# Performance work log

Measured on AMD Instinct MI355X. Metric: run time of the kernel, lower is better.

The kernel has to match this reference:

```python
import jax, jax.numpy as jnp
import numpy as np

ALPHA = 50.0
EPS = 1e-12  # torch F.normalize eps


def setup_inputs() -> dict:
    key = jax.random.key(0)
    k1, k2 = jax.random.split(key)
    N, C, H, W_sp, K = 64, 128, 64, 64, 64
    x = jax.random.normal(k1, (N, C, H, W_sp), dtype=jnp.float32)
    # centroids.permute(1,0): shape [C, K]; orthogonal-ish init approximated by scaled gaussian
    W = jax.random.normal(k2, (C, K), dtype=jnp.float32) * (1.0 / np.sqrt(C))
    bias = jnp.zeros((K,), dtype=jnp.float32)
    return {"x": x, "W": W, "bias": bias}


def _l2norm(v, axis):
    return v / jnp.maximum(jnp.linalg.norm(v, axis=axis, keepdims=True), EPS)


def reference(x, W, bias):
    N, C, H, W_sp = x.shape
    K = W.shape[1]
    x = _l2norm(x, axis=1)                      # normalize over channels
    xf = x.reshape(N, C, H * W_sp)              # [N, C, P]
    Wn = _l2norm(W, axis=0)                     # column-normalized weight [C, K]
    # soft assignment logits, computed directly in [N, K, P] layout
    sa_logits = jnp.einsum('ncp,ck->nkp', xf, Wn)
    sa = jax.nn.softmax((sa_logits + bias[None, :, None]) * ALPHA, axis=1)  # over clusters
    # VLAD via two GEMM-like contractions instead of the [N,K,C,P] residual tensor:
    # vlad[n,k,c] = sum_p sa[n,k,p] * xf[n,c,p] - W[c,k] * sum_p sa[n,k,p]
    vlad = jnp.einsum('nkp,ncp->nkc', sa, xf) - sa.sum(axis=-1)[:, :, None] * W.T[None]
    vlad = _l2norm(vlad, axis=2)                # intra-normalize per cluster
    vlad = vlad.reshape(N, K * C)
    vlad = _l2norm(vlad, axis=1)                # global L2
    return (vlad, sa_logits)                    # original returns soft_assign_ permuted to [N, K, P]
```

## Files before the change

kernel.cpp:

```cpp
#include <hip/hip_runtime.h>
#include <math.h>

#define ALPHA 50.0f
#define EPS 1e-12f

constexpr int N = 64, C = 128, P = 4096, K = 64;
constexpr int NCH2 = 8;

typedef short short8_t __attribute__((ext_vector_type(8)));
typedef short short4_t __attribute__((ext_vector_type(4)));
typedef float f4 __attribute__((ext_vector_type(4)));
typedef unsigned int u32x4 __attribute__((ext_vector_type(4)));
typedef unsigned int u32x2 __attribute__((ext_vector_type(2)));

__device__ __forceinline__ unsigned short f2bf(float f) {
    union { float f; unsigned u; } v; v.f = f;
    unsigned r = (v.u + 0x7FFFu + ((v.u >> 16) & 1u)) >> 16;
    return (unsigned short)r;
}

__device__ __forceinline__ unsigned cvtpk(float lo, float hi) {
    unsigned r;
    asm("v_cvt_pk_bf16_f32 %0, %1, %2" : "=v"(r) : "v"(lo), "v"(hi));
    return r;
}

__device__ __forceinline__ void bar_lds() {
    asm volatile("s_waitcnt lgkmcnt(0)" ::: "memory");
    __builtin_amdgcn_s_barrier();
}

__global__ __launch_bounds__(256, 2) void k_fused(
    const float* __restrict__ x, const float* __restrict__ W,
    const float* __restrict__ bias, float* __restrict__ logits,
    float* __restrict__ vlad_part, float* __restrict__ Spart,
    float* __restrict__ ss2acc)
{
    __shared__ __align__(16) char smem[71424];
    unsigned short* xsT  = (unsigned short*)smem;
    float*          saf  = (float*)smem;
    unsigned short* sa2s = (unsigned short*)(smem + 56320);
    float*          denom= (float*)(smem + 65536);
    float*          invs = (float*)(smem + 69888);
    float*          biass= (float*)(smem + 70144);
    float*          red  = (float*)(smem + 70400);
    float*          Wl   = (float*)smem;

    const int tid  = threadIdx.x;
    const int n    = blockIdx.x >> 3;
    const int blk8 = blockIdx.x & 7;
    const int pbase = blk8 * 512;

    const int w = tid >> 6, lane = tid & 63;
    const int q = lane >> 4, l15 = lane & 15;
    const int pxg = tid & 15, cg = tid >> 4;

    if (blockIdx.x == 0 && tid < 64) ss2acc[tid] = 0.f;
    if (tid < K) biass[tid] = bias[tid] * ALPHA;

    const float* xrow = x + (size_t)n * C * P + pbase + 4 * pxg;
    float4 va[8], vb[8];
    short8_t af[4];

    {
        float4 wv[8];
        #pragma unroll
        for (int it = 0; it < 8; ++it)
            wv[it] = *(const float4*)&W[(size_t)(tid + it * 256) * 4];
        #pragma unroll
        for (int j = 0; j < 8; ++j)
            va[j] = *(const float4*)&xrow[(size_t)(8 * cg + j) * P];
        #pragma unroll
        for (int it = 0; it < 8; ++it) {
            const int idx4 = tid + it * 256;
            *(float4*)&Wl[(idx4 >> 4) * 68 + (idx4 & 15) * 4] = wv[it];
        }
        bar_lds();
        {
            const int k = tid & 63, part = tid >> 6;
            float s = 0.f;
            #pragma unroll
            for (int i = 0; i < 32; ++i) {
                float v = Wl[(part * 32 + i) * 68 + k];
                s = fmaf(v, v, s);
            }
            red[tid] = s;
        }
        bar_lds();
        if (tid < 64)
            invs[tid] = 1.0f / fmaxf(
                sqrtf(red[tid] + red[64 + tid] + red[128 + tid] + red[192 + tid]), EPS);
        bar_lds();
        {
            const float cv = invs[16 * w + l15];
            #pragma unroll
            for (int c0 = 0; c0 < 4; ++c0)
                #pragma unroll
                for (int j = 0; j < 8; ++j)
                    af[c0][j] = (short)f2bf(
                        Wl[(c0 * 32 + 8 * q + j) * 68 + 16 * w + l15] * cv);
        }
        bar_lds();
    }

    f4 acc2[8];
    #pragma unroll
    for (int ct = 0; ct < 8; ++ct) acc2[ct] = (f4){0.f, 0.f, 0.f, 0.f};
    float Sreg = 0.f;

    const int pbT8 = 8 * (cg ^ (pxg & 7));
    const int l4 = l15 >> 2;

    for (int ch = 0; ch < 8; ++ch) {
        if (ch < 7) {
            const float* xb = xrow + (ch + 1) * 64;
            #pragma unroll
            for (int j = 0; j < 8; ++j)
                vb[j] = *(const float4*)&xb[(size_t)(8 * cg + j) * P];
        }
        if (ch > 0) {
            const unsigned short* xsNr =
                (const unsigned short*)(smem + 17408 + 19456 * ((ch - 1) & 1));
            short8_t a2[2];
            #pragma unroll
            for (int kit = 0; kit < 2; ++kit)
                a2[kit] = *(const short8_t*)&sa2s[(16 * w + l15) * 72 + kit * 32 + 8 * q];
            __builtin_amdgcn_s_setprio(1);
            #pragma unroll
            for (int ct = 0; ct < 8; ++ct)
                #pragma unroll
                for (int kit = 0; kit < 2; ++kit) {
                    const unsigned short* bp = &xsNr[(ct * 16 + l15) * 76 + kit * 32 + 8 * q];
                    short4_t b0 = *(const short4_t*)bp;
                    short4_t b1 = *(const short4_t*)(bp + 4);
                    short8_t bb;
                    bb[0] = b0[0]; bb[1] = b0[1]; bb[2] = b0[2]; bb[3] = b0[3];
                    bb[4] = b1[0]; bb[5] = b1[1]; bb[6] = b1[2]; bb[7] = b1[3];
                    acc2[ct] = __builtin_amdgcn_mfma_f32_16x16x32_bf16(a2[kit], bb, acc2[ct], 0, 0, 0);
                }
            __builtin_amdgcn_s_setprio(0);
        }
        {
            unsigned short* xsNw = (unsigned short*)(smem + 17408 + 19456 * (ch & 1));
            const float* vf = (const float*)va;
            float pss[4] = {0.f, 0.f, 0.f, 0.f};
            #pragma unroll
            for (int j = 0; j < 8; ++j)
                #pragma unroll
                for (int i = 0; i < 4; ++i)
                    pss[i] = fmaf(vf[j * 4 + i], vf[j * 4 + i], pss[i]);
            float* rd2 = denom;
            #pragma unroll
            for (int i = 0; i < 4; ++i) rd2[(4 * pxg + i) * 17 + cg] = pss[i];

            #pragma unroll
            for (int i = 0; i < 4; ++i) {
                u32x4 t;
                #pragma unroll
                for (int jj = 0; jj < 4; ++jj)
                    t[jj] = cvtpk(vf[(2 * jj) * 4 + i], vf[(2 * jj + 1) * 4 + i]);
                *(u32x4*)&xsT[(4 * pxg + i) * 136 + pbT8] = t;
            }
            #pragma unroll
            for (int j = 0; j < 8; ++j) {
                u32x2 t2;
                t2[0] = cvtpk(vf[j * 4 + 0], vf[j * 4 + 1]);
                t2[1] = cvtpk(vf[j * 4 + 2], vf[j * 4 + 3]);
                *(u32x2*)&xsNw[(8 * cg + j) * 76 + 4 * pxg] = t2;
            }
        }
        bar_lds();

        if (tid < 64) {
            const float* rd2 = denom;
            float s = 0.f;
            #pragma unroll
            for (int g = 0; g < 16; ++g) s += rd2[tid * 17 + g];
            invs[tid] = 1.0f / fmaxf(sqrtf(s), EPS);
        }
        f4 acc1[4];
        #pragma unroll
        for (int t = 0; t < 4; ++t) acc1[t] = (f4){0.f, 0.f, 0.f, 0.f};
        __builtin_amdgcn_s_setprio(1);
        #pragma unroll
        for (int c0 = 0; c0 < 4; ++c0)
            #pragma unroll
            for (int pxt = 0; pxt < 4; ++pxt) {
                const int pb = (4 * c0 + q) ^ (4 * (pxt & 1) + l4);
                short8_t bf = *(const short8_t*)&xsT[(pxt * 16 + l15) * 136 + pb * 8];
                acc1[pxt] = __builtin_amdgcn_mfma_f32_16x16x32_bf16(af[c0], bf, acc1[pxt], 0, 0, 0);
            }
        __builtin_amdgcn_s_setprio(0);
        bar_lds();

        {
            const int p0 = pbase + ch * 64;
            float* lgp = logits + (size_t)n * K * P + p0;
            float bz[4];
            #pragma unroll
            for (int r = 0; r < 4; ++r) bz[r] = biass[16 * w + 4 * q + r];
            #pragma unroll
            for (int pxt = 0; pxt < 4; ++pxt) {
                const int pxl = pxt * 16 + l15;
                const float iv = invs[pxl];
                float psum = 0.f;
                #pragma unroll
                for (int r = 0; r < 4; ++r) {
                    const int k = 16 * w + 4 * q + r;
                    const float lv = acc1[pxt][r] * iv;
                    __builtin_nontemporal_store(lv, &lgp[(size_t)k * P + pxl]);
                    const float e = __expf(fmaf(lv, ALPHA, bz[r]));
                    saf[k * 68 + pxl] = e;
                    psum += e;
                }
                denom[(4 * w + q) * 68 + pxl] = psum;
            }
        }
        bar_lds();

        {
            float dinv = 0.f;
            if (lane < 16) {
                const int pxr = 16 * w + lane;
                float dd = 0.f;
                #pragma unroll
                for (int g = 0; g < 16; ++g) dd += denom[g * 68 + pxr];
                dinv = 1.0f / dd;
            }
            const float* sp = &saf[lane * 68 + 16 * w];
            const float* ip = &invs[16 * w];
            float s = 0.f;
            unsigned pk[8];
            #pragma unroll
            for (int m = 0; m < 4; ++m) {
                f4 e  = *(const f4*)&sp[4 * m];
                f4 iv = *(const f4*)&ip[4 * m];
                const float r0 = __shfl(dinv, 4 * m + 0);
                const float r1 = __shfl(dinv, 4 * m + 1);
                const float r2 = __shfl(dinv, 4 * m + 2);
                const float r3 = __shfl(dinv, 4 * m + 3);
                s += e[0] * r0; s += e[1] * r1;
                s += e[2] * r2; s += e[3] * r3;
                const float v0 = e[0] * (r0 * iv[0]);
                const float v1 = e[1] * (r1 * iv[1]);
                const float v2 = e[2] * (r2 * iv[2]);
                const float v3 = e[3] * (r3 * iv[3]);
                pk[2 * m]     = cvtpk(v0, v1);
                pk[2 * m + 1] = cvtpk(v2, v3);
            }
            Sreg += s;
            *(u32x4*)&sa2s[lane * 72 + 16 * w]     = (u32x4){pk[0], pk[1], pk[2], pk[3]};
            *(u32x4*)&sa2s[lane * 72 + 16 * w + 8] = (u32x4){pk[4], pk[5], pk[6], pk[7]};
        }
        bar_lds();

        if (ch < 7) {
            #pragma unroll
            for (int j = 0; j < 8; ++j) va[j] = vb[j];
        }
    }

    {
        const unsigned short* xsNr = (const unsigned short*)(smem + 17408 + 19456 * 1);
        short8_t a2[2];
        #pragma unroll
        for (int kit = 0; kit < 2; ++kit)
            a2[kit] = *(const short8_t*)&sa2s[(16 * w + l15) * 72 + kit * 32 + 8 * q];
        __builtin_amdgcn_s_setprio(1);
        #pragma unroll
        for (int ct = 0; ct < 8; ++ct)
            #pragma unroll
            for (int kit = 0; kit < 2; ++kit) {
                const unsigned short* bp = &xsNr[(ct * 16 + l15) * 76 + kit * 32 + 8 * q];
                short4_t b0 = *(const short4_t*)bp;
                short4_t b1 = *(const short4_t*)(bp + 4);
                short8_t bb;
                bb[0] = b0[0]; bb[1] = b0[1]; bb[2] = b0[2]; bb[3] = b0[3];
                bb[4] = b1[0]; bb[5] = b1[1]; bb[6] = b1[2]; bb[7] = b1[3];
                acc2[ct] = __builtin_amdgcn_mfma_f32_16x16x32_bf16(a2[kit], bb, acc2[ct], 0, 0, 0);
            }
        __builtin_amdgcn_s_setprio(0);
    }

    float* vp = vlad_part + ((size_t)blk8 * N + n) * (size_t)(K * C);
    #pragma unroll
    for (int ct = 0; ct < 8; ++ct)
        #pragma unroll
        for (int r = 0; r < 4; ++r)
            vp[(16 * w + 4 * q + r) * C + ct * 16 + l15] = acc2[ct][r];

    red[tid] = Sreg;
    __syncthreads();
    if (tid < 64)
        Spart[((size_t)blk8 * N + n) * K + tid] =
            red[tid] + red[64 + tid] + red[128 + tid] + red[192 + tid];
}

__global__ __launch_bounds__(256) void k_post1(
    const float* __restrict__ vlad_part, const float* __restrict__ W,
    const float* __restrict__ Spart, float* __restrict__ out,
    float* __restrict__ ss2acc)
{
    __shared__ float red[16];
    const int tid = threadIdx.x;
    const int n  = blockIdx.x >> 2;
    const int kq = blockIdx.x & 3;
    const int kl = tid >> 4;
    const int ci = tid & 15;
    const int k  = kq * 16 + kl;
    const int c0 = ci * 8;

    float Sk = 0.f;
    #pragma unroll
    for (int ch = 0; ch < NCH2; ++ch) Sk += Spart[(size_t)(ch * N + n) * K + k];

    float v[8];
    #pragma unroll
    for (int l = 0; l < 8; ++l) v[l] = 0.f;
    #pragma unroll
    for (int ch = 0; ch < NCH2; ++ch) {
        const float* vp = vlad_part + ((size_t)(ch * N + n) * K + k) * C + c0;
        float4 a = *(const float4*)&vp[0];
        float4 b = *(const float4*)&vp[4];
        v[0] += a.x; v[1] += a.y; v[2] += a.z; v[3] += a.w;
        v[4] += b.x; v[5] += b.y; v[6] += b.z; v[7] += b.w;
    }

    float ss = 0.f;
    #pragma unroll
    for (int l = 0; l < 8; ++l) {
        float val = v[l] - W[(size_t)(c0 + l) * K + k] * Sk;
        v[l] = val;
        ss = fmaf(val, val, ss);
    }
    ss += __shfl_xor(ss, 1);
    ss += __shfl_xor(ss, 2);
    ss += __shfl_xor(ss, 4);
    ss += __shfl_xor(ss, 8);
    const float inv1 = 1.0f / fmaxf(sqrtf(ss), EPS);
    float ss2 = 0.f;
    #pragma unroll
    for (int l = 0; l < 8; ++l) { v[l] *= inv1; ss2 = fmaf(v[l], v[l], ss2); }
    ss2 += __shfl_xor(ss2, 1);
    ss2 += __shfl_xor(ss2, 2);
    ss2 += __shfl_xor(ss2, 4);
    ss2 += __shfl_xor(ss2, 8);
    if (ci == 0) red[kl] = ss2;
    __syncthreads();
    if (tid == 0) {
        float t = 0.f;
        #pragma unroll
        for (int i = 0; i < 16; ++i) t += red[i];
        atomicAdd(&ss2acc[n], t);
    }

    float* op = out + (size_t)n * K * C + (size_t)k * C + c0;
    *(float4*)&op[0] = (float4){v[0], v[1], v[2], v[3]};
    *(float4*)&op[4] = (float4){v[4], v[5], v[6], v[7]};
}

__global__ __launch_bounds__(256) void k_post2(
    float* __restrict__ out, const float* __restrict__ ss2acc)
{
    const int n   = blockIdx.x >> 2;
    const int seg = blockIdx.x & 3;
    const float inv2 = 1.0f / fmaxf(sqrtf(ss2acc[n]), EPS);
    float* p = out + (size_t)n * K * C + (size_t)seg * 2048 + (size_t)threadIdx.x * 8;
    float4 a = *(const float4*)&p[0];
    float4 b = *(const float4*)&p[4];
    a.x *= inv2; a.y *= inv2; a.z *= inv2; a.w *= inv2;
    b.x *= inv2; b.y *= inv2; b.z *= inv2; b.w *= inv2;
    *(float4*)&p[0] = a;
    *(float4*)&p[4] = b;
}

extern "C" void kernel_launch(void* const* d_in, const int* in_sizes, int n_in,
                              void* d_out, int out_size, void* d_ws, size_t ws_size,
                              hipStream_t stream)
{
    const float* x    = (const float*)d_in[0];
    const float* W    = (const float*)d_in[1];
    const float* bias = (const float*)d_in[2];

    float* out_vlad   = (float*)d_out;
    float* out_logits = (float*)d_out + (size_t)N * K * C;

    float* ss2acc     = (float*)((char*)d_ws + 16384);
    float* Spart      = (float*)((char*)d_ws + 32768);
    float* vlad_part  = (float*)((char*)d_ws + 32768 + 131072);

    k_fused<<<dim3(N * NCH2), dim3(256), 0, stream>>>(
        x, W, bias, out_logits, vlad_part, Spart, ss2acc);
    k_post1<<<dim3(N * 4), dim3(256), 0, stream>>>(vlad_part, W, Spart, out_vlad, ss2acc);
    k_post2<<<dim3(N * 4), dim3(256), 0, stream>>>(out_vlad, ss2acc);
}
```

Baseline: 235.9 us.

## Split fused NetVLAD block across 8 waves with per-wave K/C tile halves

```diff
diff --git a/kernel.cpp b/kernel.cpp
--- a/kernel.cpp
+++ b/kernel.cpp
@@ -30,21 +30,23 @@
     __builtin_amdgcn_s_barrier();
 }
 
-__global__ __launch_bounds__(256, 2) void k_fused(
+__global__ __launch_bounds__(512, 4) void k_fused(
     const float* __restrict__ x, const float* __restrict__ W,
     const float* __restrict__ bias, float* __restrict__ logits,
     float* __restrict__ vlad_part, float* __restrict__ Spart,
     float* __restrict__ ss2acc)
 {
-    __shared__ __align__(16) char smem[71424];
+    __shared__ __align__(16) char smem[72704];
     unsigned short* xsT  = (unsigned short*)smem;
-    float*          saf  = (float*)smem;
-    unsigned short* sa2s = (unsigned short*)(smem + 56320);
-    float*          denom= (float*)(smem + 65536);
-    float*          invs = (float*)(smem + 69888);
-    float*          biass= (float*)(smem + 70144);
-    float*          red  = (float*)(smem + 70400);
+    unsigned short* xsN  = (unsigned short*)(smem + 17408);
+    float*          saf  = (float*)(smem + 36864);
+    unsigned short* sa2s = (unsigned short*)(smem + 54272);
+    float*          denom= (float*)(smem + 63488);
+    float*          invs = (float*)(smem + 72192);
+    float*          biass= (float*)(smem + 72448);
     float*          Wl   = (float*)smem;
+    float*          rd2  = denom;
+    float*          red  = denom;
 
     const int tid  = threadIdx.x;
     const int n    = blockIdx.x >> 3;
@@ -52,162 +54,150 @@
     const int pbase = blk8 * 512;
 
     const int w = tid >> 6, lane = tid & 63;
-    const int q = lane >> 4, l15 = lane & 15;
-    const int pxg = tid & 15, cg = tid >> 4;
+    const int q = lane >> 4, l15 = lane & 15, l4 = l15 >> 2;
+    const int kt = w >> 1, h = w & 1;
+    const int pxg = tid & 15, cgrp = tid >> 4;
 
     if (blockIdx.x == 0 && tid < 64) ss2acc[tid] = 0.f;
-    if (tid < K) biass[tid] = bias[tid] * ALPHA;
 
     const float* xrow = x + (size_t)n * C * P + pbase + 4 * pxg;
-    float4 va[8], vb[8];
+    float4 va[4], vb[4];
     short8_t af[4];
+    float bz[4];
 
     {
-        float4 wv[8];
-        #pragma unroll
-        for (int it = 0; it < 8; ++it)
-            wv[it] = *(const float4*)&W[(size_t)(tid + it * 256) * 4];
-        #pragma unroll
-        for (int j = 0; j < 8; ++j)
-            va[j] = *(const float4*)&xrow[(size_t)(8 * cg + j) * P];
-        #pragma unroll
-        for (int it = 0; it < 8; ++it) {
-            const int idx4 = tid + it * 256;
-            *(float4*)&Wl[(idx4 >> 4) * 68 + (idx4 & 15) * 4] = wv[it];
-        }
-        bar_lds();
-        {
-            const int k = tid & 63, part = tid >> 6;
+        #pragma unroll
+        for (int j = 0; j < 4; ++j)
+            va[j] = *(const float4*)&xrow[(size_t)(4 * cgrp + j) * P];
+        if (tid < K) biass[tid] = bias[tid] * ALPHA;
+        #pragma unroll
+        for (int pass = 0; pass < 2; ++pass) {
+            float4 wv[4];
+            #pragma unroll
+            for (int it = 0; it < 4; ++it)
+                wv[it] = *(const float4*)&W[(size_t)(tid + (4 * pass + it) * 512) * 4];
+            #pragma unroll
+            for (int it = 0; it < 4; ++it) {
+                const int idx4 = tid + (4 * pass + it) * 512;
+                *(float4*)&Wl[(idx4 >> 4) * 68 + (idx4 & 15) * 4] = wv[it];
+            }
+        }
+        bar_lds();
+        {
             float s = 0.f;
             #pragma unroll
-            for (int i = 0; i < 32; ++i) {
-                float v = Wl[(part * 32 + i) * 68 + k];
+            for (int i = 0; i < 16; ++i) {
+                float v = Wl[(w * 16 + i) * 68 + lane];
                 s = fmaf(v, v, s);
             }
             red[tid] = s;
         }
         bar_lds();
-        if (tid < 64)
-            invs[tid] = 1.0f / fmaxf(
-                sqrtf(red[tid] + red[64 + tid] + red[128 + tid] + red[192 + tid]), EPS);
-        bar_lds();
-        {
-            const float cv = invs[16 * w + l15];
+        if (tid < 64) {
+            float s = 0.f;
+            #pragma unroll
+            for (int p = 0; p < 8; ++p) s += red[64 * p + tid];
+            invs[tid] = 1.0f / fmaxf(sqrtf(s), EPS);
+        }
+        bar_lds();
+        {
+            const float cv = invs[16 * kt + l15];
             #pragma unroll
             for (int c0 = 0; c0 < 4; ++c0)
                 #pragma unroll
                 for (int j = 0; j < 8; ++j)
                     af[c0][j] = (short)f2bf(
-                        Wl[(c0 * 32 + 8 * q + j) * 68 + 16 * w + l15] * cv);
-        }
-        bar_lds();
-    }
-
-    f4 acc2[8];
-    #pragma unroll
-    for (int ct = 0; ct < 8; ++ct) acc2[ct] = (f4){0.f, 0.f, 0.f, 0.f};
+                        Wl[(c0 * 32 + 8 * q + j) * 68 + 16 * kt + l15] * cv);
+            #pragma unroll
+            for (int r = 0; r < 4; ++r) bz[r] = biass[16 * kt + 4 * q + r];
+        }
+        bar_lds();
+    }
+
+    f4 acc2[4];
+    #pragma unroll
+    for (int ct = 0; ct < 4; ++ct) acc2[ct] = (f4){0.f, 0.f, 0.f, 0.f};
     float Sreg = 0.f;
 
-    const int pbT8 = 8 * (cg ^ (pxg & 7));
-    const int l4 = l15 >> 2;
+    const int pbT = (cgrp >> 1) ^ (pxg & 7);
 
     for (int ch = 0; ch < 8; ++ch) {
         if (ch < 7) {
             const float* xb = xrow + (ch + 1) * 64;
             #pragma unroll
-            for (int j = 0; j < 8; ++j)
-                vb[j] = *(const float4*)&xb[(size_t)(8 * cg + j) * P];
-        }
-        if (ch > 0) {
-            const unsigned short* xsNr =
-                (const unsigned short*)(smem + 17408 + 19456 * ((ch - 1) & 1));
-            short8_t a2[2];
-            #pragma unroll
-            for (int kit = 0; kit < 2; ++kit)
-                a2[kit] = *(const short8_t*)&sa2s[(16 * w + l15) * 72 + kit * 32 + 8 * q];
-            __builtin_amdgcn_s_setprio(1);
-            #pragma unroll
-            for (int ct = 0; ct < 8; ++ct)
-                #pragma unroll
-                for (int kit = 0; kit < 2; ++kit) {
-                    const unsigned short* bp = &xsNr[(ct * 16 + l15) * 76 + kit * 32 + 8 * q];
-                    short4_t b0 = *(const short4_t*)bp;
-                    short4_t b1 = *(const short4_t*)(bp + 4);
-                    short8_t bb;
-                    bb[0] = b0[0]; bb[1] = b0[1]; bb[2] = b0[2]; bb[3] = b0[3];
-                    bb[4] = b1[0]; bb[5] = b1[1]; bb[6] = b1[2]; bb[7] = b1[3];
-                    acc2[ct] = __builtin_amdgcn_mfma_f32_16x16x32_bf16(a2[kit], bb, acc2[ct], 0, 0, 0);
-                }
-            __builtin_amdgcn_s_setprio(0);
-        }
-        {
-            unsigned short* xsNw = (unsigned short*)(smem + 17408 + 19456 * (ch & 1));
-            const float* vf = (const float*)va;
+            for (int j = 0; j < 4; ++j)
+                vb[j] = *(const float4*)&xb[(size_t)(4 * cgrp + j) * P];
+        }
+        bar_lds();
+        const float* vf = (const float*)va;
+
+        {
             float pss[4] = {0.f, 0.f, 0.f, 0.f};
             #pragma unroll
-            for (int j = 0; j < 8; ++j)
+            for (int j = 0; j < 4; ++j)
                 #pragma unroll
                 for (int i = 0; i < 4; ++i)
                     pss[i] = fmaf(vf[j * 4 + i], vf[j * 4 + i], pss[i]);
-            float* rd2 = denom;
-            #pragma unroll
-            for (int i = 0; i < 4; ++i) rd2[(4 * pxg + i) * 17 + cg] = pss[i];
+            #pragma unroll
+            for (int i = 0; i < 4; ++i) rd2[(4 * pxg + i) * 33 + cgrp] = pss[i];
 
             #pragma unroll
             for (int i = 0; i < 4; ++i) {
-                u32x4 t;
-                #pragma unroll
-                for (int jj = 0; jj < 4; ++jj)
-                    t[jj] = cvtpk(vf[(2 * jj) * 4 + i], vf[(2 * jj + 1) * 4 + i]);
-                *(u32x4*)&xsT[(4 * pxg + i) * 136 + pbT8] = t;
-            }
-            #pragma unroll
-            for (int j = 0; j < 8; ++j) {
+                u32x2 t2;
+                t2[0] = cvtpk(vf[0 * 4 + i], vf[1 * 4 + i]);
+                t2[1] = cvtpk(vf[2 * 4 + i], vf[3 * 4 + i]);
+                *(u32x2*)&xsT[(4 * pxg + i) * 136 + pbT * 8 + (cgrp & 1) * 4] = t2;
+            }
+            #pragma unroll
+            for (int j = 0; j < 4; ++j) {
                 u32x2 t2;
                 t2[0] = cvtpk(vf[j * 4 + 0], vf[j * 4 + 1]);
                 t2[1] = cvtpk(vf[j * 4 + 2], vf[j * 4 + 3]);
-                *(u32x2*)&xsNw[(8 * cg + j) * 76 + 4 * pxg] = t2;
-            }
-        }
-        bar_lds();
-
-        if (tid < 64) {
-            const float* rd2 = denom;
+                *(u32x2*)&xsN[(4 * cgrp + j) * 76 + 4 * pxg] = t2;
+            }
+        }
+        bar_lds();
+
+        float myinv = 0.f;
+        {
+            const int pxL = h * 32 + ((lane >> 4) & 1) * 16 + l15;
+            const int gb  = (lane >> 5) * 16;
             float s = 0.f;
             #pragma unroll
-            for (int g = 0; g < 16; ++g) s += rd2[tid * 17 + g];
-            invs[tid] = 1.0f / fmaxf(sqrtf(s), EPS);
-        }
-        f4 acc1[4];
-        #pragma unroll
-        for (int t = 0; t < 4; ++t) acc1[t] = (f4){0.f, 0.f, 0.f, 0.f};
+            for (int g = 0; g < 16; ++g) s += rd2[pxL * 33 + gb + g];
+            s += __shfl_xor(s, 32);
+            myinv = 1.0f / fmaxf(sqrtf(s), EPS);
+            if (lane < 32) invs[pxL] = myinv;
+        }
+        f4 acc1[2];
+        acc1[0] = (f4){0.f, 0.f, 0.f, 0.f};
+        acc1[1] = (f4){0.f, 0.f, 0.f, 0.f};
         __builtin_amdgcn_s_setprio(1);
         #pragma unroll
         for (int c0 = 0; c0 < 4; ++c0)
             #pragma unroll
-            for (int pxt = 0; pxt < 4; ++pxt) {
-                const int pb = (4 * c0 + q) ^ (4 * (pxt & 1) + l4);
+            for (int p2 = 0; p2 < 2; ++p2) {
+                const int pxt = 2 * h + p2;
+                const int pb = (4 * c0 + q) ^ (4 * p2 + l4);
                 short8_t bf = *(const short8_t*)&xsT[(pxt * 16 + l15) * 136 + pb * 8];
-                acc1[pxt] = __builtin_amdgcn_mfma_f32_16x16x32_bf16(af[c0], bf, acc1[pxt], 0, 0, 0);
+                acc1[p2] = __builtin_amdgcn_mfma_f32_16x16x32_bf16(af[c0], bf, acc1[p2], 0, 0, 0);
             }
         __builtin_amdgcn_s_setprio(0);
-        bar_lds();
-
         {
             const int p0 = pbase + ch * 64;
             float* lgp = logits + (size_t)n * K * P + p0;
-            float bz[4];
-            #pragma unroll
-            for (int r = 0; r < 4; ++r) bz[r] = biass[16 * w + 4 * q + r];
-            #pragma unroll
-            for (int pxt = 0; pxt < 4; ++pxt) {
-                const int pxl = pxt * 16 + l15;
-                const float iv = invs[pxl];
+            float ivv[2];
+            ivv[0] = __shfl(myinv, l15);
+            ivv[1] = __shfl(myinv, 16 + l15);
+            #pragma unroll
+            for (int p2 = 0; p2 < 2; ++p2) {
+                const int pxl = (2 * h + p2) * 16 + l15;
+                const float iv = ivv[p2];
                 float psum = 0.f;
                 #pragma unroll
                 for (int r = 0; r < 4; ++r) {
-                    const int k = 16 * w + 4 * q + r;
-                    const float lv = acc1[pxt][r] * iv;
+                    const int k = 16 * kt + 4 * q + r;
+                    const float lv = acc1[p2][r] * iv;
                     __builtin_nontemporal_store(lv, &lgp[(size_t)k * P + pxl]);
                     const float e = __expf(fmaf(lv, ALPHA, bz[r]));
                     saf[k * 68 + pxl] = e;
@@ -220,21 +210,26 @@
 
         {
             float dinv = 0.f;
-            if (lane < 16) {
-                const int pxr = 16 * w + lane;
+            if (lane < 8) {
+                const int px = 8 * w + lane;
+                const int H = px >> 5;
                 float dd = 0.f;
                 #pragma unroll
-                for (int g = 0; g < 16; ++g) dd += denom[g * 68 + pxr];
+                for (int t = 0; t < 4; ++t)
+                    #pragma unroll
+                    for (int qq = 0; qq < 4; ++qq)
+                        dd += denom[(8 * t + 4 * H + qq) * 68 + px];
                 dinv = 1.0f / dd;
             }
-            const float* sp = &saf[lane * 68 + 16 * w];
-            const float* ip = &invs[16 * w];
+            const float* sp = &saf[lane * 68 + 8 * w];
+            const f4 ivA = *(const f4*)&invs[8 * w];
+            const f4 ivB = *(const f4*)&invs[8 * w + 4];
             float s = 0.f;
-            unsigned pk[8];
-            #pragma unroll
-            for (int m = 0; m < 4; ++m) {
-                f4 e  = *(const f4*)&sp[4 * m];
-                f4 iv = *(const f4*)&ip[4 * m];
+            unsigned pk[4];
+            #pragma unroll
+            for (int m = 0; m < 2; ++m) {
+                f4 e = *(const f4*)&sp[4 * m];
+                const f4 iv = m ? ivB : ivA;
                 const float r0 = __shfl(dinv, 4 * m + 0);
                 const float r1 = __shfl(dinv, 4 * m + 1);
                 const float r2 = __shfl(dinv, 4 * m + 2);
@@ -249,51 +244,55 @@
                 pk[2 * m + 1] = cvtpk(v2, v3);
             }
             Sreg += s;
-            *(u32x4*)&sa2s[lane * 72 + 16 * w]     = (u32x4){pk[0], pk[1], pk[2], pk[3]};
-            *(u32x4*)&sa2s[lane * 72 + 16 * w + 8] = (u32x4){pk[4], pk[5], pk[6], pk[7]};
-        }
-        bar_lds();
+            *(u32x4*)&sa2s[lane * 72 + 8 * w] = (u32x4){pk[0], pk[1], pk[2], pk[3]};
+        }
+        bar_lds();
+
+        {
+            short8_t a2[2];
+            #pragma unroll
+            for (int kit = 0; kit < 2; ++kit)
+                a2[kit] = *(const short8_t*)&sa2s[(16 * kt + l15) * 72 + kit * 32 + 8 * q];
+            __builtin_amdgcn_s_setprio(1);
+            #pragma unroll
+            for (int ctl = 0; ctl < 4; ++ctl) {
+                const int ct = 4 * h + ctl;
+                #pragma unroll
+                for (int kit = 0; kit < 2; ++kit) {
+                    const unsigned short* bp = &xsN[(ct * 16 + l15) * 76 + kit * 32 + 8 * q];
+                    short4_t b0 = *(const short4_t*)bp;
+                    short4_t b1 = *(const short4_t*)(bp + 4);
+                    short8_t bb;
+                    bb[0] = b0[0]; bb[1] = b0[1]; bb[2] = b0[2]; bb[3] = b0[3];
+                    bb[4] = b1[0]; bb[5] = b1[1]; bb[6] = b1[2]; bb[7] = b1[3];
+                    acc2[ctl] = __builtin_amdgcn_mfma_f32_16x16x32_bf16(a2[kit], bb, acc2[ctl], 0, 0, 0);
+                }
+            }
+            __builtin_amdgcn_s_setprio(0);
+        }
 
         if (ch < 7) {
             #pragma unroll
-            for (int j = 0; j < 8; ++j) va[j] = vb[j];
-        }
-    }
-
-    {
-        const unsigned short* xsNr = (const unsigned short*)(smem + 17408 + 19456 * 1);
-        short8_t a2[2];
-        #pragma unroll
-        for (int kit = 0; kit < 2; ++kit)
-            a2[kit] = *(const short8_t*)&sa2s[(16 * w + l15) * 72 + kit * 32 + 8 * q];
-        __builtin_amdgcn_s_setprio(1);
-        #pragma unroll
-        for (int ct = 0; ct < 8; ++ct)
-            #pragma unroll
-            for (int kit = 0; kit < 2; ++kit) {
-                const unsigned short* bp = &xsNr[(ct * 16 + l15) * 76 + kit * 32 + 8 * q];
-                short4_t b0 = *(const short4_t*)bp;
-                short4_t b1 = *(const short4_t*)(bp + 4);
-                short8_t bb;
-                bb[0] = b0[0]; bb[1] = b0[1]; bb[2] = b0[2]; bb[3] = b0[3];
-                bb[4] = b1[0]; bb[5] = b1[1]; bb[6] = b1[2]; bb[7] = b1[3];
-                acc2[ct] = __builtin_amdgcn_mfma_f32_16x16x32_bf16(a2[kit], bb, acc2[ct], 0, 0, 0);
-            }
-        __builtin_amdgcn_s_setprio(0);
+            for (int j = 0; j < 4; ++j) va[j] = vb[j];
+        }
     }
 
     float* vp = vlad_part + ((size_t)blk8 * N + n) * (size_t)(K * C);
     #pragma unroll
-    for (int ct = 0; ct < 8; ++ct)
+    for (int ctl = 0; ctl < 4; ++ctl)
         #pragma unroll
         for (int r = 0; r < 4; ++r)
-            vp[(16 * w + 4 * q + r) * C + ct * 16 + l15] = acc2[ct][r];
-
+            vp[(16 * kt + 4 * q + r) * C + (4 * h + ctl) * 16 + l15] = acc2[ctl][r];
+
+    __syncthreads();
     red[tid] = Sreg;
     __syncthreads();
-    if (tid < 64)
-        Spart[((size_t)blk8 * N + n) * K + tid] =
-            red[tid] + red[64 + tid] + red[128 + tid] + red[192 + tid];
+    if (tid < 64) {
+        float s = 0.f;
+        #pragma unroll
+        for (int p = 0; p < 8; ++p) s += red[64 * p + tid];
+        Spart[((size_t)blk8 * N + n) * K + tid] = s;
+    }
 }
 
 __global__ __launch_bounds__(256) void k_post1(
@@ -389,7 +388,7 @@
     float* Spart      = (float*)((char*)d_ws + 32768);
     float* vlad_part  = (float*)((char*)d_ws + 32768 + 131072);
 
-    k_fused<<<dim3(N * NCH2), dim3(256), 0, stream>>>(
+    k_fused<<<dim3(N * NCH2), dim3(512), 0, stream>>>(
         x, W, bias, out_logits, vlad_part, Spart, ss2acc);
     k_post1<<<dim3(N * 4), dim3(256), 0, stream>>>(vlad_part, W, Spart, out_vlad, ss2acc);
     k_post2<<<dim3(N * 4), dim3(256), 0, stream>>>(out_vlad, ss2acc);
```

Result: slower. 245.2 us (+4.0%).
